# Kernel tuning notes

Hardware: AMD Instinct MI355X
Metric: run time of the kernel (lower is better)

## Reference

```python
import jax, jax.numpy as jnp
import numpy as np

L, R = -0.1, 1.1          # HardKuma stretched support
MAX_REL = 11              # max relative distance
CLAMP_LO, CLAMP_HI = 0.01, 100.0


def setup_inputs() -> dict:
    key = jax.random.key(0)
    ks = jax.random.split(key, 12)
    B, T, Din, Dout = 4, 2048, 512, 256
    s_in = 0.02
    return {
        "q": jax.random.normal(ks[0], (B, T, Din), jnp.float32),
        "k": jax.random.normal(ks[1], (B, T, Din), jnp.float32),
        "Wa1": jax.random.normal(ks[2], (Din, Dout), jnp.float32) * s_in,
        "ba1": jnp.zeros((Dout,), jnp.float32),
        "Wa2": jax.random.normal(ks[3], (Dout, Dout), jnp.float32) * s_in,
        "ba2": jnp.zeros((Dout,), jnp.float32),
        "Wb1": jax.random.normal(ks[4], (Din, Dout), jnp.float32) * s_in,
        "bb1": jnp.zeros((Dout,), jnp.float32),
        "Wb2": jax.random.normal(ks[5], (Dout, Dout), jnp.float32) * s_in,
        "bb2": jnp.zeros((Dout,), jnp.float32),
        "dist_emb": jax.random.normal(ks[6], (2 * MAX_REL + 1,), jnp.float32) * 0.02,
    }


def _mlp(x, W1, b1, W2, b2):
    # Sequential(Linear, ReLU, Dropout, Linear, ReLU, Dropout) in eval mode
    h = jax.nn.relu(x @ W1 + b1)
    return jax.nn.relu(h @ W2 + b2)


def _rel_dists(T, dist_emb):
    i = jnp.arange(T)
    rel = jnp.clip(i[None, :] - i[:, None], -MAX_REL, MAX_REL) + MAX_REL  # [T,T] ints in [0,22]
    return dist_emb[rel]  # [T,T]


def _kuma_cdf(t, a, b):
    # F(t; a, b) = 1 - (1 - t^a)^b, t is a positive Python-float constant
    return 1.0 - jnp.power(1.0 - jnp.power(t, a), b)


def _kuma_mean(a, b):
    # E[X] = b * Beta(1 + 1/a, b)
    g = 1.0 + 1.0 / a
    return b * jnp.exp(jax.scipy.special.gammaln(g) + jax.scipy.special.gammaln(b)
                       - jax.scipy.special.gammaln(g + b))


def reference(q, k, Wa1, ba1, Wa2, ba2, Wb1, bb1, Wb2, bb2, dist_emb):
    T = q.shape[1]
    q_a = _mlp(q, Wa1, ba1, Wa2, ba2)
    k_a = _mlp(k, Wa1, ba1, Wa2, ba2)
    q_b = _mlp(q, Wb1, bb1, Wb2, bb2)
    k_b = _mlp(k, Wb1, bb1, Wb2, bb2)

    a = jnp.einsum("btd,bsd->bts", q_a, k_a)  # [B,T,T]
    b = jnp.einsum("btd,bsd->bts", q_b, k_b)

    rd = _rel_dists(T, dist_emb)[None]  # [1,T,T]
    a = a + rd
    b = b + rd

    a = jnp.clip(jax.nn.softplus(a), CLAMP_LO, CLAMP_HI)
    b = jnp.clip(jax.nn.softplus(b), CLAMP_LO, CLAMP_HI)

    # HardKuma deterministic (eval) attention
    t0 = (0.0 - L) / (R - L)  # stretched coord of 0
    t1 = (1.0 - L) / (R - L)  # stretched coord of 1
    p0 = _kuma_cdf(t0, a, b)          # P(h = 0)
    p1 = 1.0 - _kuma_cdf(t1, a, b)    # P(h = 1)
    pc = 1.0 - p0 - p1                # continuous mass

    mean = jnp.clip(L + (R - L) * _kuma_mean(a, b), 0.0, 1.0)
    zero_one = jnp.where(p0 > p1, 0.0, 1.0)
    att = jnp.where(pc < 0.5, zero_one, mean)
    return att
```

## Files before the change

kernel.cpp:

```cpp
#include <hip/hip_runtime.h>
#include <hip/hip_bf16.h>
#include <math.h>

typedef __hip_bfloat16 bf16;
typedef short bf16x8 __attribute__((ext_vector_type(8)));
typedef float f32x4 __attribute__((ext_vector_type(4)));
typedef float f32x2 __attribute__((ext_vector_type(2)));

union alignas(16) Pack8 { bf16 h[8]; bf16x8 v; };

#define EXP2F(x) __builtin_amdgcn_exp2f(x)
#define LOG2F(x) __builtin_amdgcn_logf(x)
#define RCPF(x)  __builtin_amdgcn_rcpf(x)

#define TAB_N   64
#define TAB_LO  (-0.35f)
#define TAB_HI  (1.25f)
#define TAB_STRIDE 65

__global__ void prep_weights(const float* __restrict__ Wa1, const float* __restrict__ Wa2,
                             const float* __restrict__ Wb1, const float* __restrict__ Wb2,
                             bf16* __restrict__ oa1, bf16* __restrict__ oa2,
                             bf16* __restrict__ ob1, bf16* __restrict__ ob2) {
    int idx = blockIdx.x * 256 + threadIdx.x;
    if (idx < 131072) {
        int n = idx >> 9, k = idx & 511;
        oa1[idx] = __float2bfloat16(Wa1[k * 256 + n]);
    } else if (idx < 196608) {
        int i = idx - 131072; int n = i >> 8, k = i & 255;
        oa2[i] = __float2bfloat16(Wa2[k * 256 + n]);
    } else if (idx < 327680) {
        int i = idx - 196608; int n = i >> 9, k = i & 511;
        ob1[i] = __float2bfloat16(Wb1[k * 256 + n]);
    } else {
        int i = idx - 327680; int n = i >> 8, k = i & 255;
        ob2[i] = __float2bfloat16(Wb2[k * 256 + n]);
    }
}

__device__ __forceinline__ float stirl2s(float z) {
    float iz = 1.f / z;
    return (z - 0.5f) * LOG2F(z) - 1.44269504f * z + 1.32574806f
         + iz * (0.12022651f - 0.00400749f * iz * iz);
}
__device__ __forceinline__ float sp4s(float x) {
    return (x * (x + 1.f)) * ((x + 2.f) * (x + 3.f));
}
__device__ float mean_f32(float sa, float sb) {
    float lw = LOG2F(1.f + EXP2F(sa * 1.44269504f));
    float lv = LOG2F(1.f + EXP2F(sb * 1.44269504f));
    lw = fminf(fmaxf(lw, 0.01442695f), 144.269504f);
    lv = fminf(fmaxf(lv, 0.01442695f), 144.269504f);
    float b = 0.69314718f * lv;
    float g = 1.44269504f / lw + 1.f;
    float gb = g + b;
    float lb2 = stirl2s(g + 4.f) + stirl2s(b + 4.f) - stirl2s(gb + 4.f)
              + LOG2F(sp4s(gb) / (sp4s(g) * sp4s(b)));
    float mean = fmaf(1.2f * b, EXP2F(lb2), -0.1f);
    return fminf(fmaxf(mean, 0.f), 1.f);
}

__global__ void gen_table(float* __restrict__ tab) {
    int idx = blockIdx.x * 256 + threadIdx.x;
    if (idx >= TAB_N * TAB_N) return;
    int ia = idx >> 6, ib = idx & 63;
    const float step = (TAB_HI - TAB_LO) / (TAB_N - 1);
    float sa  = TAB_LO + ia * step;
    float sb  = TAB_LO + ib * step;
    int ib1 = ib < TAB_N - 1 ? ib + 1 : ib;
    float sb1 = TAB_LO + ib1 * step;
    tab[(ia * TAB_STRIDE + ib) * 2]     = mean_f32(sa, sb);
    tab[(ia * TAB_STRIDE + ib) * 2 + 1] = mean_f32(sa, sb1);
}

__global__ __launch_bounds__(256, 2)
void mlp_fused(const float* __restrict__ q, const float* __restrict__ k,
               const bf16* __restrict__ Wa1t, const bf16* __restrict__ Wa2t,
               const bf16* __restrict__ Wb1t, const bf16* __restrict__ Wb2t,
               bf16* __restrict__ qa, bf16* __restrict__ ka,
               bf16* __restrict__ qb, bf16* __restrict__ kb) {
    const int z = blockIdx.z;
    const float* X  = (z & 1) ? k : q;
    const bf16*  W1 = (z >> 1) ? Wb1t : Wa1t;
    const bf16*  W2 = (z >> 1) ? Wb2t : Wa2t;
    bf16* Y = (z == 0) ? qa : (z == 1) ? ka : (z == 2) ? qb : kb;
    const int m0 = blockIdx.x * 64;

    __shared__ short lA[64 * 40];
    __shared__ short lB[256 * 40];
    __shared__ short lH[64 * 264];

    const int tid  = threadIdx.x;
    const int wave = tid >> 6, lane = tid & 63;
    const int wn = wave * 64;
    const int quad = lane >> 4, r16 = lane & 15;

    {
        f32x4 acc[4][4] = {};
        for (int kk = 0; kk < 512; kk += 32) {
            {
                int r = tid >> 2, c = (tid & 3) * 8;
                const float* p = X + (size_t)(m0 + r) * 512 + kk + c;
                Pack8 u;
#pragma unroll
                for (int j = 0; j < 8; j++) u.h[j] = __float2bfloat16(p[j]);
                *(bf16x8*)&lA[r * 40 + c] = u.v;
            }
            for (int i = tid; i < 1024; i += 256) {
                int r = i >> 2, c = (i & 3) * 8;
                *(bf16x8*)&lB[r * 40 + c] =
                    *(const bf16x8*)(W1 + (size_t)r * 512 + kk + c);
            }
            __syncthreads();
            bf16x8 af[4], bfr[4];
#pragma unroll
            for (int f = 0; f < 4; f++) {
                af[f]  = *(const bf16x8*)&lA[(f * 16 + r16) * 40 + quad * 8];
                bfr[f] = *(const bf16x8*)&lB[(wn + f * 16 + r16) * 40 + quad * 8];
            }
#pragma unroll
            for (int i = 0; i < 4; i++)
#pragma unroll
                for (int j = 0; j < 4; j++)
                    acc[i][j] = __builtin_amdgcn_mfma_f32_16x16x32_bf16(
                        af[i], bfr[j], acc[i][j], 0, 0, 0);
            __syncthreads();
        }
#pragma unroll
        for (int i = 0; i < 4; i++)
#pragma unroll
            for (int j = 0; j < 4; j++)
#pragma unroll
                for (int r = 0; r < 4; r++) {
                    float v = acc[i][j][r];
                    v = v > 0.f ? v : 0.f;
                    ((bf16*)lH)[(i * 16 + quad * 4 + r) * 264 + wn + j * 16 + r16] =
                        __float2bfloat16(v);
                }
    }
    __syncthreads();

    f32x4 acc2[4][4] = {};
    for (int kk = 0; kk < 256; kk += 32) {
        for (int i = tid; i < 1024; i += 256) {
            int r = i >> 2, c = (i & 3) * 8;
            *(bf16x8*)&lB[r * 40 + c] =
                *(const bf16x8*)(W2 + (size_t)r * 256 + kk + c);
        }
        __syncthreads();
        bf16x8 af[4], bfr[4];
#pragma unroll
        for (int f = 0; f < 4; f++) {
            af[f]  = *(const bf16x8*)&lH[(f * 16 + r16) * 264 + kk + quad * 8];
            bfr[f] = *(const bf16x8*)&lB[(wn + f * 16 + r16) * 40 + quad * 8];
        }
#pragma unroll
        for (int i = 0; i < 4; i++)
#pragma unroll
            for (int j = 0; j < 4; j++)
                acc2[i][j] = __builtin_amdgcn_mfma_f32_16x16x32_bf16(
                    af[i], bfr[j], acc2[i][j], 0, 0, 0);
        __syncthreads();
    }

#pragma unroll
    for (int i = 0; i < 4; i++) {
        int rbase = m0 + i * 16 + quad * 4;
#pragma unroll
        for (int j = 0; j < 4; j++) {
            int col = wn + j * 16 + r16;
#pragma unroll
            for (int r = 0; r < 4; r++) {
                float v = acc2[i][j][r];
                v = v > 0.f ? v : 0.f;
                Y[(size_t)(rbase + r) * 256 + col] = __float2bfloat16(v);
            }
        }
    }
}

__device__ __forceinline__ f32x2 vexp2(f32x2 x) {
    f32x2 r; r.x = EXP2F(x.x); r.y = EXP2F(x.y); return r;
}
__device__ __forceinline__ f32x2 vlog2(f32x2 x) {
    f32x2 r; r.x = LOG2F(x.x); r.y = LOG2F(x.y); return r;
}
__device__ __forceinline__ f32x2 vrcp(f32x2 x) {
    f32x2 r; r.x = RCPF(x.x); r.y = RCPF(x.y); return r;
}
__device__ __forceinline__ f32x2 vclamp(f32x2 x, float lo, float hi) {
    f32x2 r;
    r.x = fminf(fmaxf(x.x, lo), hi);
    r.y = fminf(fmaxf(x.y, lo), hi);
    return r;
}

__device__ __noinline__ f32x2 hardkuma_slow(f32x2 la, f32x2 lb) {
    const float LOG2E = 1.44269504f;
    f32x2 lw = vlog2(1.f + vexp2(la * LOG2E));
    f32x2 lv = vlog2(1.f + vexp2(lb * LOG2E));
    lw = vclamp(lw, 0.01442695f, 144.269504f);
    lv = vclamp(lv, 0.01442695f, 144.269504f);
    f32x2 b = 0.69314718f * lv;

    f32x2 t0a = vexp2(-2.48490665f * lw);
    f32x2 t1a = vexp2(-0.08701138f * lw);
    f32x2 q0 = vexp2(b * vlog2(1.f - t0a));
    f32x2 p1 = vexp2(b * vlog2(1.f - t1a));
    f32x2 pc = q0 - p1;
    f32x2 p0 = 1.f - q0;

    f32x2 g  = 1.44269504f * vrcp(lw) + 1.f;
    f32x2 gb = g + b;
    f32x2 g2 = g + 2.f, b2 = b + 2.f, gb2 = gb + 2.f;

    f32x2 s = (g + 1.5f) * vlog2(g2) + (b + 1.5f) * vlog2(b2)
            - (gb + 1.5f) * vlog2(gb2);

    const float C1 = 0.12022459f;
    const float C2 = -0.00400749f;
    f32x2 pg  = g2 * b2;
    f32x2 rr3 = vrcp(pg * gb2);
    f32x2 ig  = rr3 * (b2 * gb2);
    f32x2 ib  = rr3 * (g2 * gb2);
    f32x2 igb = rr3 * pg;
    f32x2 corr = ig  * (C1 + C2 * (ig  * ig))
               + ib  * (C1 + C2 * (ib  * ib))
               - igb * (C1 + C2 * (igb * igb));
    s += corr - 1.55964202f;

    f32x2 ng = g * (g + 1.f), nb = b * (b + 1.f), ngb = gb * (gb + 1.f);
    s += vlog2(ngb * vrcp(ng * nb));

    f32x2 mean = (1.2f * b) * vexp2(s) - 0.1f;
    mean = vclamp(mean, 0.f, 1.f);

    f32x2 att;
    att.x = (pc.x < 0.5f) ? ((p0.x > p1.x) ? 0.f : 1.f) : mean.x;
    att.y = (pc.y < 0.5f) ? ((p0.y > p1.y) ? 0.f : 1.f) : mean.y;
    return att;
}

__global__ __launch_bounds__(256, 2)
void kuma_attn(const bf16* __restrict__ qa, const bf16* __restrict__ ka,
               const bf16* __restrict__ qb, const bf16* __restrict__ kb,
               const float* __restrict__ dist_emb, const float* __restrict__ tabg,
               float* __restrict__ out) {
    const int bidx = blockIdx.z;
    const int t0 = blockIdx.x * 128;
    const int s0 = blockIdx.y * 128;

    __shared__ short lQa[128 * 40], lQb[128 * 40];
    __shared__ short lKa[128 * 40], lKb[128 * 40];
    __shared__ float sDist[23];
    __shared__ float sTab[TAB_N * TAB_STRIDE * 2];

    const int tid = threadIdx.x;
    if (tid < 23) sDist[tid] = dist_emb[tid];
    for (int i = tid; i < (TAB_N * TAB_STRIDE * 2) / 4; i += 256)
        ((f32x4*)sTab)[i] = ((const f32x4*)tabg)[i];

    const int wave = tid >> 6, lane = tid & 63;
    const int wm = (wave >> 1) * 64, wn = (wave & 1) * 64;
    const int quad = lane >> 4, r16 = lane & 15;
    const size_t base = (size_t)bidx * 2048 * 256;

    f32x4 accA[4][4] = {};
    f32x4 accB[4][4] = {};

    const int r0 = tid >> 2, c0 = (tid & 3) * 8;
    const int r1 = r0 + 64,  c1 = c0;

    for (int kk = 0; kk < 256; kk += 32) {
        {
            size_t gq0 = base + (size_t)(t0 + r0) * 256 + kk + c0;
            size_t gq1 = base + (size_t)(t0 + r1) * 256 + kk + c1;
            *(bf16x8*)&lQa[r0 * 40 + c0] = *(const bf16x8*)(qa + gq0);
            *(bf16x8*)&lQb[r0 * 40 + c0] = *(const bf16x8*)(qb + gq0);
            *(bf16x8*)&lQa[r1 * 40 + c1] = *(const bf16x8*)(qa + gq1);
            *(bf16x8*)&lQb[r1 * 40 + c1] = *(const bf16x8*)(qb + gq1);
            size_t gk0 = base + (size_t)(s0 + r0) * 256 + kk + c0;
            size_t gk1 = base + (size_t)(s0 + r1) * 256 + kk + c1;
            *(bf16x8*)&lKa[r0 * 40 + c0] = *(const bf16x8*)(ka + gk0);
            *(bf16x8*)&lKb[r0 * 40 + c0] = *(const bf16x8*)(kb + gk0);
            *(bf16x8*)&lKa[r1 * 40 + c1] = *(const bf16x8*)(ka + gk1);
            *(bf16x8*)&lKb[r1 * 40 + c1] = *(const bf16x8*)(kb + gk1);
        }
        __syncthreads();
        bf16x8 aA[4], aB[4], bA[4], bB[4];
#pragma unroll
        for (int f = 0; f < 4; f++) {
            int ar = (wm + f * 16 + r16) * 40 + quad * 8;
            aA[f] = *(const bf16x8*)&lQa[ar];
            aB[f] = *(const bf16x8*)&lQb[ar];
            int br = (wn + f * 16 + r16) * 40 + quad * 8;
            bA[f] = *(const bf16x8*)&lKa[br];
            bB[f] = *(const bf16x8*)&lKb[br];
        }
#pragma unroll
        for (int i = 0; i < 4; i++)
#pragma unroll
            for (int j = 0; j < 4; j++) {
                accA[i][j] = __builtin_amdgcn_mfma_f32_16x16x32_bf16(
                    aA[i], bA[j], accA[i][j], 0, 0, 0);
                accB[i][j] = __builtin_amdgcn_mfma_f32_16x16x32_bf16(
                    aB[i], bB[j], accB[i][j], 0, 0, 0);
            }
        __syncthreads();
    }

    const float SCALE = (TAB_N - 1) / (TAB_HI - TAB_LO);
#pragma unroll
    for (int i = 0; i < 4; i++) {
#pragma unroll
        for (int j = 0; j < 4; j++) {
            int s = s0 + wn + j * 16 + r16;
#pragma unroll
            for (int rr = 0; rr < 2; rr++) {
                int t = t0 + wm + i * 16 + quad * 4 + rr * 2;
                int d0 = s - t;
                int d1 = d0 - 1;
                d0 = d0 < -11 ? -11 : (d0 > 11 ? 11 : d0);
                d1 = d1 < -11 ? -11 : (d1 > 11 ? 11 : d1);
                float rd0 = sDist[d0 + 11];
                float rd1 = sDist[d1 + 11];
                f32x2 la  = { accA[i][j][rr * 2] + rd0, accA[i][j][rr * 2 + 1] + rd1 };
                f32x2 lbv = { accB[i][j][rr * 2] + rd0, accB[i][j][rr * 2 + 1] + rd1 };

                float mn = fminf(fminf(la.x, la.y), fminf(lbv.x, lbv.y));
                float mx = fmaxf(fmaxf(la.x, la.y), fmaxf(lbv.x, lbv.y));

                f32x2 u = vclamp((la  - TAB_LO) * SCALE, 0.f, (float)(TAB_N - 1));
                f32x2 v = vclamp((lbv - TAB_LO) * SCALE, 0.f, (float)(TAB_N - 1));
                int ia0 = (int)u.x; ia0 = ia0 > TAB_N - 2 ? TAB_N - 2 : ia0;
                int ia1 = (int)u.y; ia1 = ia1 > TAB_N - 2 ? TAB_N - 2 : ia1;
                int ib0 = (int)v.x; ib0 = ib0 > TAB_N - 2 ? TAB_N - 2 : ib0;
                int ib1 = (int)v.y; ib1 = ib1 > TAB_N - 2 ? TAB_N - 2 : ib1;
                f32x2 fa = { u.x - (float)ia0, u.y - (float)ia1 };
                f32x2 fb = { v.x - (float)ib0, v.y - (float)ib1 };
                int o0 = (ia0 * TAB_STRIDE + ib0) * 2;
                int o1 = (ia1 * TAB_STRIDE + ib1) * 2;
                f32x2 e0r0 = *(const f32x2*)&sTab[o0];
                f32x2 e0r1 = *(const f32x2*)&sTab[o0 + TAB_STRIDE * 2];
                f32x2 e1r0 = *(const f32x2*)&sTab[o1];
                f32x2 e1r1 = *(const f32x2*)&sTab[o1 + TAB_STRIDE * 2];
                f32x2 m0 = { e0r0.x + fb.x * (e0r0.y - e0r0.x),
                             e1r0.x + fb.y * (e1r0.y - e1r0.x) };
                f32x2 m1 = { e0r1.x + fb.x * (e0r1.y - e0r1.x),
                             e1r1.x + fb.y * (e1r1.y - e1r1.x) };
                f32x2 att = m0 + fa * (m1 - m0);

                bool oob = (mn < TAB_LO) | (mx > TAB_HI);
                if (__builtin_expect(__any(oob), 0)) {
                    f32x2 ex = hardkuma_slow(la, lbv);
                    if (oob) att = ex;
                }

                out[((size_t)bidx * 2048 + t) * 2048 + s] = att.x;
                out[((size_t)bidx * 2048 + t + 1) * 2048 + s] = att.y;
            }
        }
    }
}

extern "C" void kernel_launch(void* const* d_in, const int* in_sizes, int n_in,
                              void* d_out, int out_size, void* d_ws, size_t ws_size,
                              hipStream_t stream) {
    const float* q    = (const float*)d_in[0];
    const float* k    = (const float*)d_in[1];
    const float* Wa1  = (const float*)d_in[2];
    const float* Wa2  = (const float*)d_in[4];
    const float* Wb1  = (const float*)d_in[6];
    const float* Wb2  = (const float*)d_in[8];
    const float* dist = (const float*)d_in[10];
    float* out = (float*)d_out;

    bf16* wsbf = (bf16*)d_ws;
    bf16* Wa1t = wsbf;
    bf16* Wa2t = Wa1t + 131072;
    bf16* Wb1t = Wa2t + 65536;
    bf16* Wb2t = Wb1t + 131072;
    bf16* qa   = Wb2t + 65536;
    bf16* ka   = qa + 2097152;
    bf16* qb   = ka + 2097152;
    bf16* kb   = qb + 2097152;
    float* tabg = (float*)Wa1t;

    prep_weights<<<1536, 256, 0, stream>>>(Wa1, Wa2, Wb1, Wb2,
                                           Wa1t, Wa2t, Wb1t, Wb2t);

    dim3 g1(128, 1, 4), blk(256, 1, 1);
    mlp_fused<<<g1, blk, 0, stream>>>(q, k, Wa1t, Wa2t, Wb1t, Wb2t,
                                      qa, ka, qb, kb);

    gen_table<<<16, 256, 0, stream>>>(tabg);

    dim3 g2(16, 16, 4);
    kuma_attn<<<g2, blk, 0, stream>>>(qa, ka, qb, kb, dist, tabg, out);
}
```

Measured before the change: 197.0 us.

## Use 512-thread blocks for MLP and attention, fold table generation into weight prep

Doubles the wave count per block in both the MLP and attention kernels. Each wave now computes a 64x32 tile instead of 64x64, which halves accumulator registers and allows higher occupancy via launch bounds of (512,4). The lookup-table generation moves into extra blocks of the weight-prep kernel and into its own workspace region, removing one kernel launch. In exchange, the per-wave MFMA work per LDS load shrinks, and only half the threads load the A tile in the MLP.

Result: faster. 182.5 us (-7.3%).

```diff
diff --git a/kernel.cpp b/kernel.cpp
--- a/kernel.cpp
+++ b/kernel.cpp
@@ -18,10 +18,46 @@
 #define TAB_HI  (1.25f)
 #define TAB_STRIDE 65
 
+__device__ __forceinline__ float stirl2s(float z) {
+    float iz = 1.f / z;
+    return (z - 0.5f) * LOG2F(z) - 1.44269504f * z + 1.32574806f
+         + iz * (0.12022651f - 0.00400749f * iz * iz);
+}
+__device__ __forceinline__ float sp4s(float x) {
+    return (x * (x + 1.f)) * ((x + 2.f) * (x + 3.f));
+}
+__device__ float mean_f32(float sa, float sb) {
+    float lw = LOG2F(1.f + EXP2F(sa * 1.44269504f));
+    float lv = LOG2F(1.f + EXP2F(sb * 1.44269504f));
+    lw = fminf(fmaxf(lw, 0.01442695f), 144.269504f);
+    lv = fminf(fmaxf(lv, 0.01442695f), 144.269504f);
+    float b = 0.69314718f * lv;
+    float g = 1.44269504f / lw + 1.f;
+    float gb = g + b;
+    float lb2 = stirl2s(g + 4.f) + stirl2s(b + 4.f) - stirl2s(gb + 4.f)
+              + LOG2F(sp4s(gb) / (sp4s(g) * sp4s(b)));
+    float mean = fmaf(1.2f * b, EXP2F(lb2), -0.1f);
+    return fminf(fmaxf(mean, 0.f), 1.f);
+}
+
 __global__ void prep_weights(const float* __restrict__ Wa1, const float* __restrict__ Wa2,
                              const float* __restrict__ Wb1, const float* __restrict__ Wb2,
                              bf16* __restrict__ oa1, bf16* __restrict__ oa2,
-                             bf16* __restrict__ ob1, bf16* __restrict__ ob2) {
+                             bf16* __restrict__ ob1, bf16* __restrict__ ob2,
+                             float* __restrict__ tab) {
+    if (blockIdx.x >= 1536) {
+        int idx = (blockIdx.x - 1536) * 256 + threadIdx.x;
+        if (idx >= TAB_N * TAB_N) return;
+        int ia = idx >> 6, ib = idx & 63;
+        const float step = (TAB_HI - TAB_LO) / (TAB_N - 1);
+        float sa  = TAB_LO + ia * step;
+        float sb  = TAB_LO + ib * step;
+        int ib1 = ib < TAB_N - 1 ? ib + 1 : ib;
+        float sb1 = TAB_LO + ib1 * step;
+        tab[(ia * TAB_STRIDE + ib) * 2]     = mean_f32(sa, sb);
+        tab[(ia * TAB_STRIDE + ib) * 2 + 1] = mean_f32(sa, sb1);
+        return;
+    }
     int idx = blockIdx.x * 256 + threadIdx.x;
     if (idx < 131072) {
         int n = idx >> 9, k = idx & 511;
@@ -38,42 +74,7 @@
     }
 }
 
-__device__ __forceinline__ float stirl2s(float z) {
-    float iz = 1.f / z;
-    return (z - 0.5f) * LOG2F(z) - 1.44269504f * z + 1.32574806f
-         + iz * (0.12022651f - 0.00400749f * iz * iz);
-}
-__device__ __forceinline__ float sp4s(float x) {
-    return (x * (x + 1.f)) * ((x + 2.f) * (x + 3.f));
-}
-__device__ float mean_f32(float sa, float sb) {
-    float lw = LOG2F(1.f + EXP2F(sa * 1.44269504f));
-    float lv = LOG2F(1.f + EXP2F(sb * 1.44269504f));
-    lw = fminf(fmaxf(lw, 0.01442695f), 144.269504f);
-    lv = fminf(fmaxf(lv, 0.01442695f), 144.269504f);
-    float b = 0.69314718f * lv;
-    float g = 1.44269504f / lw + 1.f;
-    float gb = g + b;
-    float lb2 = stirl2s(g + 4.f) + stirl2s(b + 4.f) - stirl2s(gb + 4.f)
-              + LOG2F(sp4s(gb) / (sp4s(g) * sp4s(b)));
-    float mean = fmaf(1.2f * b, EXP2F(lb2), -0.1f);
-    return fminf(fmaxf(mean, 0.f), 1.f);
-}
-
-__global__ void gen_table(float* __restrict__ tab) {
-    int idx = blockIdx.x * 256 + threadIdx.x;
-    if (idx >= TAB_N * TAB_N) return;
-    int ia = idx >> 6, ib = idx & 63;
-    const float step = (TAB_HI - TAB_LO) / (TAB_N - 1);
-    float sa  = TAB_LO + ia * step;
-    float sb  = TAB_LO + ib * step;
-    int ib1 = ib < TAB_N - 1 ? ib + 1 : ib;
-    float sb1 = TAB_LO + ib1 * step;
-    tab[(ia * TAB_STRIDE + ib) * 2]     = mean_f32(sa, sb);
-    tab[(ia * TAB_STRIDE + ib) * 2 + 1] = mean_f32(sa, sb1);
-}
-
-__global__ __launch_bounds__(256, 2)
+__global__ __launch_bounds__(512, 4)
 void mlp_fused(const float* __restrict__ q, const float* __restrict__ k,
                const bf16* __restrict__ Wa1t, const bf16* __restrict__ Wa2t,
                const bf16* __restrict__ Wb1t, const bf16* __restrict__ Wb2t,
@@ -92,13 +93,13 @@
 
     const int tid  = threadIdx.x;
     const int wave = tid >> 6, lane = tid & 63;
-    const int wn = wave * 64;
+    const int wn = wave * 32;
     const int quad = lane >> 4, r16 = lane & 15;
 
     {
-        f32x4 acc[4][4] = {};
+        f32x4 acc[4][2] = {};
         for (int kk = 0; kk < 512; kk += 32) {
-            {
+            if (tid < 256) {
                 int r = tid >> 2, c = (tid & 3) * 8;
                 const float* p = X + (size_t)(m0 + r) * 512 + kk + c;
                 Pack8 u;
@@ -106,22 +107,23 @@
                 for (int j = 0; j < 8; j++) u.h[j] = __float2bfloat16(p[j]);
                 *(bf16x8*)&lA[r * 40 + c] = u.v;
             }
-            for (int i = tid; i < 1024; i += 256) {
+            for (int i = tid; i < 1024; i += 512) {
                 int r = i >> 2, c = (i & 3) * 8;
                 *(bf16x8*)&lB[r * 40 + c] =
                     *(const bf16x8*)(W1 + (size_t)r * 512 + kk + c);
             }
             __syncthreads();
-            bf16x8 af[4], bfr[4];
-#pragma unroll
-            for (int f = 0; f < 4; f++) {
-                af[f]  = *(const bf16x8*)&lA[(f * 16 + r16) * 40 + quad * 8];
+            bf16x8 af[4], bfr[2];
+#pragma unroll
+            for (int f = 0; f < 4; f++)
+                af[f] = *(const bf16x8*)&lA[(f * 16 + r16) * 40 + quad * 8];
+#pragma unroll
+            for (int f = 0; f < 2; f++)
                 bfr[f] = *(const bf16x8*)&lB[(wn + f * 16 + r16) * 40 + quad * 8];
-            }
 #pragma unroll
             for (int i = 0; i < 4; i++)
 #pragma unroll
-                for (int j = 0; j < 4; j++)
+                for (int j = 0; j < 2; j++)
                     acc[i][j] = __builtin_amdgcn_mfma_f32_16x16x32_bf16(
                         af[i], bfr[j], acc[i][j], 0, 0, 0);
             __syncthreads();
@@ -129,7 +131,7 @@
 #pragma unroll
         for (int i = 0; i < 4; i++)
 #pragma unroll
-            for (int j = 0; j < 4; j++)
+            for (int j = 0; j < 2; j++)
 #pragma unroll
                 for (int r = 0; r < 4; r++) {
                     float v = acc[i][j][r];
@@ -140,24 +142,25 @@
     }
     __syncthreads();
 
-    f32x4 acc2[4][4] = {};
+    f32x4 acc2[4][2] = {};
     for (int kk = 0; kk < 256; kk += 32) {
-        for (int i = tid; i < 1024; i += 256) {
+        for (int i = tid; i < 1024; i += 512) {
             int r = i >> 2, c = (i & 3) * 8;
             *(bf16x8*)&lB[r * 40 + c] =
                 *(const bf16x8*)(W2 + (size_t)r * 256 + kk + c);
         }
         __syncthreads();
-        bf16x8 af[4], bfr[4];
-#pragma unroll
-        for (int f = 0; f < 4; f++) {
-            af[f]  = *(const bf16x8*)&lH[(f * 16 + r16) * 264 + kk + quad * 8];
+        bf16x8 af[4], bfr[2];
+#pragma unroll
+        for (int f = 0; f < 4; f++)
+            af[f] = *(const bf16x8*)&lH[(f * 16 + r16) * 264 + kk + quad * 8];
+#pragma unroll
+        for (int f = 0; f < 2; f++)
             bfr[f] = *(const bf16x8*)&lB[(wn + f * 16 + r16) * 40 + quad * 8];
-        }
 #pragma unroll
         for (int i = 0; i < 4; i++)
 #pragma unroll
-            for (int j = 0; j < 4; j++)
+            for (int j = 0; j < 2; j++)
                 acc2[i][j] = __builtin_amdgcn_mfma_f32_16x16x32_bf16(
                     af[i], bfr[j], acc2[i][j], 0, 0, 0);
         __syncthreads();
@@ -167,7 +170,7 @@
     for (int i = 0; i < 4; i++) {
         int rbase = m0 + i * 16 + quad * 4;
 #pragma unroll
-        for (int j = 0; j < 4; j++) {
+        for (int j = 0; j < 2; j++) {
             int col = wn + j * 16 + r16;
 #pragma unroll
             for (int r = 0; r < 4; r++) {
@@ -241,7 +244,7 @@
     return att;
 }
 
-__global__ __launch_bounds__(256, 2)
+__global__ __launch_bounds__(512, 4)
 void kuma_attn(const bf16* __restrict__ qa, const bf16* __restrict__ ka,
                const bf16* __restrict__ qb, const bf16* __restrict__ kb,
                const float* __restrict__ dist_emb, const float* __restrict__ tabg,
@@ -257,42 +260,39 @@
 
     const int tid = threadIdx.x;
     if (tid < 23) sDist[tid] = dist_emb[tid];
-    for (int i = tid; i < (TAB_N * TAB_STRIDE * 2) / 4; i += 256)
+    for (int i = tid; i < (TAB_N * TAB_STRIDE * 2) / 4; i += 512)
         ((f32x4*)sTab)[i] = ((const f32x4*)tabg)[i];
 
     const int wave = tid >> 6, lane = tid & 63;
-    const int wm = (wave >> 1) * 64, wn = (wave & 1) * 64;
+    const int wm = (wave >> 2) * 64;
+    const int wn = (wave & 3) * 32;
     const int quad = lane >> 4, r16 = lane & 15;
     const size_t base = (size_t)bidx * 2048 * 256;
 
-    f32x4 accA[4][4] = {};
-    f32x4 accB[4][4] = {};
+    f32x4 accA[4][2] = {};
+    f32x4 accB[4][2] = {};
 
     const int r0 = tid >> 2, c0 = (tid & 3) * 8;
-    const int r1 = r0 + 64,  c1 = c0;
 
     for (int kk = 0; kk < 256; kk += 32) {
         {
-            size_t gq0 = base + (size_t)(t0 + r0) * 256 + kk + c0;
-            size_t gq1 = base + (size_t)(t0 + r1) * 256 + kk + c1;
-            *(bf16x8*)&lQa[r0 * 40 + c0] = *(const bf16x8*)(qa + gq0);
-            *(bf16x8*)&lQb[r0 * 40 + c0] = *(const bf16x8*)(qb + gq0);
-            *(bf16x8*)&lQa[r1 * 40 + c1] = *(const bf16x8*)(qa + gq1);
-            *(bf16x8*)&lQb[r1 * 40 + c1] = *(const bf16x8*)(qb + gq1);
-            size_t gk0 = base + (size_t)(s0 + r0) * 256 + kk + c0;
-            size_t gk1 = base + (size_t)(s0 + r1) * 256 + kk + c1;
-            *(bf16x8*)&lKa[r0 * 40 + c0] = *(const bf16x8*)(ka + gk0);
-            *(bf16x8*)&lKb[r0 * 40 + c0] = *(const bf16x8*)(kb + gk0);
-            *(bf16x8*)&lKa[r1 * 40 + c1] = *(const bf16x8*)(ka + gk1);
-            *(bf16x8*)&lKb[r1 * 40 + c1] = *(const bf16x8*)(kb + gk1);
+            size_t gq = base + (size_t)(t0 + r0) * 256 + kk + c0;
+            size_t gk = base + (size_t)(s0 + r0) * 256 + kk + c0;
+            *(bf16x8*)&lQa[r0 * 40 + c0] = *(const bf16x8*)(qa + gq);
+            *(bf16x8*)&lQb[r0 * 40 + c0] = *(const bf16x8*)(qb + gq);
+            *(bf16x8*)&lKa[r0 * 40 + c0] = *(const bf16x8*)(ka + gk);
+            *(bf16x8*)&lKb[r0 * 40 + c0] = *(const bf16x8*)(kb + gk);
         }
         __syncthreads();
-        bf16x8 aA[4], aB[4], bA[4], bB[4];
+        bf16x8 aA[4], aB[4], bA[2], bB[2];
 #pragma unroll
         for (int f = 0; f < 4; f++) {
             int ar = (wm + f * 16 + r16) * 40 + quad * 8;
             aA[f] = *(const bf16x8*)&lQa[ar];
             aB[f] = *(const bf16x8*)&lQb[ar];
+        }
+#pragma unroll
+        for (int f = 0; f < 2; f++) {
             int br = (wn + f * 16 + r16) * 40 + quad * 8;
             bA[f] = *(const bf16x8*)&lKa[br];
             bB[f] = *(const bf16x8*)&lKb[br];
@@ -300,7 +300,7 @@
 #pragma unroll
         for (int i = 0; i < 4; i++)
 #pragma unroll
-            for (int j = 0; j < 4; j++) {
+            for (int j = 0; j < 2; j++) {
                 accA[i][j] = __builtin_amdgcn_mfma_f32_16x16x32_bf16(
                     aA[i], bA[j], accA[i][j], 0, 0, 0);
                 accB[i][j] = __builtin_amdgcn_mfma_f32_16x16x32_bf16(
@@ -313,7 +313,7 @@
 #pragma unroll
     for (int i = 0; i < 4; i++) {
 #pragma unroll
-        for (int j = 0; j < 4; j++) {
+        for (int j = 0; j < 2; j++) {
             int s = s0 + wn + j * 16 + r16;
 #pragma unroll
             for (int rr = 0; rr < 2; rr++) {
@@ -384,17 +384,16 @@
     bf16* ka   = qa + 2097152;
     bf16* qb   = ka + 2097152;
     bf16* kb   = qb + 2097152;
-    float* tabg = (float*)Wa1t;
-
-    prep_weights<<<1536, 256, 0, stream>>>(Wa1, Wa2, Wb1, Wb2,
-                                           Wa1t, Wa2t, Wb1t, Wb2t);
-
-    dim3 g1(128, 1, 4), blk(256, 1, 1);
-    mlp_fused<<<g1, blk, 0, stream>>>(q, k, Wa1t, Wa2t, Wb1t, Wb2t,
-                                      qa, ka, qb, kb);
-
-    gen_table<<<16, 256, 0, stream>>>(tabg);
+    bf16* tail = kb + 2097152;
+    float* tabg = (float*)tail;
+
+    prep_weights<<<1552, 256, 0, stream>>>(Wa1, Wa2, Wb1, Wb2,
+                                           Wa1t, Wa2t, Wb1t, Wb2t, tabg);
+
+    dim3 g1(128, 1, 4), blk512(512, 1, 1);
+    mlp_fused<<<g1, blk512, 0, stream>>>(q, k, Wa1t, Wa2t, Wb1t, Wb2t,
+                                         qa, ka, qb, kb);
 
     dim3 g2(16, 16, 4);
-    kuma_attn<<<g2, blk, 0, stream>>>(qa, ka, qb, kb, dist, tabg, out);
-}
+    kuma_attn<<<g2, blk512, 0, stream>>>(qa, ka, qb, kb, dist, tabg, out);
+}
```
